# Performance work log

Hardware: AMD Instinct MI355X
Metric: run time of the kernel (lower is better)

## Reference

```python
import jax, jax.numpy as jnp
import numpy as np
import math

L, V, D, H, TBLK = 12, 50257, 768, 12, 1024
HD = D // H
EPS = 1e-5


def setup_inputs() -> dict:
    key = jax.random.key(0)
    ks = jax.random.split(key, 16)
    B, T = 2, 1024
    s = 0.02
    idx = jax.random.randint(ks[0], (B, T), 0, V, dtype=jnp.int32)
    inp = {
        "idx": idx,
        "wte": jax.random.normal(ks[1], (V, D), jnp.float32) * s,
        "wpe": jax.random.normal(ks[2], (TBLK, D), jnp.float32) * s,
        # per-layer params stacked along leading L axis
        "ln1_g": jnp.ones((L, D), jnp.float32),
        "ln1_b": jnp.zeros((L, D), jnp.float32),
        "attn_w": jax.random.normal(ks[3], (L, D, 3 * D), jnp.float32) * s,
        "attn_b": jnp.zeros((L, 3 * D), jnp.float32),
        "aproj_w": jax.random.normal(ks[4], (L, D, D), jnp.float32) * s,
        "aproj_b": jnp.zeros((L, D), jnp.float32),
        "ln2_g": jnp.ones((L, D), jnp.float32),
        "ln2_b": jnp.zeros((L, D), jnp.float32),
        "fc_w": jax.random.normal(ks[5], (L, D, 4 * D), jnp.float32) * s,
        "fc_b": jnp.zeros((L, 4 * D), jnp.float32),
        "mproj_w": jax.random.normal(ks[6], (L, 4 * D, D), jnp.float32) * s,
        "mproj_b": jnp.zeros((L, D), jnp.float32),
        "lnf_g": jnp.ones((D,), jnp.float32),
        "lnf_b": jnp.zeros((D,), jnp.float32),
        "lm_w": jax.random.normal(ks[7], (D, V), jnp.float32) * s,  # lm_head weight (stored transposed)
    }
    return inp


def _layer_norm(x, g, b):
    mu = jnp.mean(x, axis=-1, keepdims=True)
    var = jnp.mean(jnp.square(x - mu), axis=-1, keepdims=True)
    return (x - mu) * jax.lax.rsqrt(var + EPS) * g + b


def _block(x, p):
    (ln1g, ln1b, aw, ab, pw, pb, ln2g, ln2b, fw, fb, mw, mb) = p
    B, T, C = x.shape
    h = _layer_norm(x, ln1g, ln1b)
    qkv = h @ aw + ab  # [B,T,3D]
    q, k, v = jnp.split(qkv, 3, axis=-1)
    q = q.reshape(B, T, H, HD)
    k = k.reshape(B, T, H, HD)
    v = v.reshape(B, T, H, HD)
    scores = jnp.einsum('bihd,bjhd->bhij', q, k) * (1.0 / math.sqrt(HD))
    mask = jnp.tril(jnp.ones((T, T), bool))
    scores = jnp.where(mask, scores, jnp.float32(-jnp.inf))
    attn = jax.nn.softmax(scores, axis=-1)
    o = jnp.einsum('bhij,bjhd->bihd', attn, v).reshape(B, T, C)
    x = x + o @ pw + pb
    h = _layer_norm(x, ln2g, ln2b)
    h = jax.nn.gelu(h @ fw + fb, approximate=True)
    x = x + h @ mw + mb
    return x, None


def reference(idx, wte, wpe, ln1_g, ln1_b, attn_w, attn_b, aproj_w, aproj_b,
              ln2_g, ln2_b, fc_w, fc_b, mproj_w, mproj_b, lnf_g, lnf_b, lm_w):
    B, T = idx.shape
    x = wte[idx] + wpe[jnp.arange(T)]
    layers = (ln1_g, ln1_b, attn_w, attn_b, aproj_w, aproj_b,
              ln2_g, ln2_b, fc_w, fc_b, mproj_w, mproj_b)
    x, _ = jax.lax.scan(_block, x, layers)
    x = _layer_norm(x, lnf_g, lnf_b)
    logits = x @ lm_w  # [B,T,V]
    return logits
```

## Files before the change

### kernel.cpp

```cpp
#include <hip/hip_runtime.h>
#include <hip/hip_bf16.h>
#include <math.h>

#define BT_   2048
#define D_    768
#define T_    1024
#define H_    12
#define HD_   64
#define L_    12
#define V_    50257
#define VPAD_ 50304
#define NCHUNK_ 7168

typedef __hip_bfloat16 bf16;
typedef short bf16x8 __attribute__((ext_vector_type(8)));
typedef float f32x4 __attribute__((ext_vector_type(4)));

__global__ __launch_bounds__(256) void embed_kernel(const int* __restrict__ idx,
                                                    const float* __restrict__ wte,
                                                    const float* __restrict__ wpe,
                                                    float* __restrict__ x) {
    int bt = blockIdx.x;
    int t  = bt & (T_ - 1);
    int tok = idx[bt];
    const float* wrow = wte + (size_t)tok * D_;
    const float* prow = wpe + (size_t)t * D_;
    float* xrow = x + (size_t)bt * D_;
    for (int d = threadIdx.x; d < D_; d += 256)
        xrow[d] = wrow[d] + prow[d];
}

__global__ __launch_bounds__(256) void lnorm_kernel(const float* __restrict__ in,
                                                    const float* __restrict__ g,
                                                    const float* __restrict__ b,
                                                    bf16* __restrict__ out) {
    int row = blockIdx.x;
    const float* xr = in + (size_t)row * D_;
    float s = 0.f, s2 = 0.f;
    for (int d = threadIdx.x; d < D_; d += 256) {
        float v = xr[d];
        s += v; s2 += v * v;
    }
    #pragma unroll
    for (int o = 32; o >= 1; o >>= 1) {
        s  += __shfl_xor(s,  o);
        s2 += __shfl_xor(s2, o);
    }
    __shared__ float ss[4], ss2[4];
    int wid = threadIdx.x >> 6;
    if ((threadIdx.x & 63) == 0) { ss[wid] = s; ss2[wid] = s2; }
    __syncthreads();
    s  = ss[0] + ss[1] + ss[2] + ss[3];
    s2 = ss2[0] + ss2[1] + ss2[2] + ss2[3];
    float mu  = s / D_;
    float var = s2 / D_ - mu * mu;
    float rstd = rsqrtf(var + 1e-5f);
    bf16* orow = out + (size_t)row * D_;
    for (int d = threadIdx.x; d < D_; d += 256)
        orow[d] = __float2bfloat16((xr[d] - mu) * rstd * g[d] + b[d]);
}

__global__ __launch_bounds__(256) void convT_kernel(const float* __restrict__ W,
                                                    bf16* __restrict__ Wt,
                                                    int K, int ldW, int n_src0, int Nreal,
                                                    size_t sW, size_t sT) {
    W  += (size_t)blockIdx.z * sW;
    Wt += (size_t)blockIdx.z * sT;
    __shared__ float t[32][33];
    int tx = threadIdx.x & 31, ty = threadIdx.x >> 5;
    int k0 = blockIdx.y * 32, n0 = blockIdx.x * 32;
    #pragma unroll
    for (int i = 0; i < 4; i++) {
        int k = k0 + ty + i * 8;
        int n = n_src0 + n0 + tx;
        t[ty + i * 8][tx] = (n < Nreal) ? W[(size_t)k * ldW + n] : 0.f;
    }
    __syncthreads();
    #pragma unroll
    for (int i = 0; i < 4; i++)
        Wt[(size_t)(n0 + ty + i * 8) * K + k0 + tx] = __float2bfloat16(t[tx][ty + i * 8]);
}

__device__ inline float gelu_f(float v) {
    const float c = 0.7978845608028654f;
    float u = c * (v + 0.044715f * v * v * v);
    return 0.5f * v * (1.f + tanhf(u));
}

__device__ inline void gload16(const void* g, void* l) {
    __builtin_amdgcn_global_load_lds((const __attribute__((address_space(1))) void*)g,
                                     (__attribute__((address_space(3))) void*)l, 16, 0, 0);
}

template <int BM, int BN, int WM, int WN, int EPI, typename OT>
__device__ __attribute__((always_inline)) void gemm_body(
        const bf16* __restrict__ A, const bf16* __restrict__ Bt,
        const float* __restrict__ bias, const float* res, OT* C,
        int K, int ldC, int n_off, int Ncap, int nx) {
    constexpr int NW = WM * WN;
    constexpr int MI = BM / WM / 16;
    constexpr int NJ = BN / WN / 16;
    constexpr int GA = (BM / 16) / NW;
    constexpr int GB = (BN / 16) / NW;
    constexpr int G  = GA + GB;
    static_assert(GA >= 1 && GB >= 1, "stage mapping needs >=1 seg per wave");
    __shared__ __align__(16) short smem[3 * (BM + BN) * 32];
    short* Asm = smem;
    short* Bsm = smem + 3 * BM * 32;
    const int tid  = threadIdx.x;
    const int lane = tid & 63;
    const int wid  = tid >> 6;
    const int wm = wid / WN, wn = wid % WN;

    const int nwg = gridDim.x;
    const int bid = blockIdx.x;
    const int q8  = nwg >> 3, r8 = nwg & 7;
    const int xcd = bid & 7, off = bid >> 3;
    const int swz = (xcd < r8 ? xcd * (q8 + 1) : r8 * (q8 + 1) + (xcd - r8) * q8) + off;
    const int m0 = (swz % nx) * BM;
    const int n0 = (swz / nx) * BN;

    const int rS = lane >> 2;
    const int cS = ((lane & 3) ^ ((lane >> 3) & 3)) * 8;
    const int fr = lane & 15;
    const int fq = lane >> 4;
    const int rc = (fq ^ ((fr >> 1) & 3)) * 8;

    auto STAGE = [&](int buf, int k0) {
        #pragma unroll
        for (int s = 0; s < GA; s++) {
            const int seg = wid * GA + s;
            gload16(A + (size_t)(m0 + seg * 16 + rS) * K + k0 + cS, &Asm[buf * BM * 32 + seg * 512]);
        }
        #pragma unroll
        for (int s = 0; s < GB; s++) {
            const int seg = wid * GB + s;
            gload16(Bt + (size_t)(n0 + seg * 16 + rS) * K + k0 + cS, &Bsm[buf * BN * 32 + seg * 512]);
        }
    };

    f32x4 acc[MI][NJ] = {};

    auto COMPUTE = [&](int buf) {
        bf16x8 af[MI], bfr[NJ];
        #pragma unroll
        for (int i = 0; i < MI; i++)
            af[i] = *(const bf16x8*)&Asm[buf * BM * 32 + (wm * (BM / WM) + i * 16 + fr) * 32 + rc];
        #pragma unroll
        for (int j = 0; j < NJ; j++)
            bfr[j] = *(const bf16x8*)&Bsm[buf * BN * 32 + (wn * (BN / WN) + j * 16 + fr) * 32 + rc];
        #pragma unroll
        for (int i = 0; i < MI; i++)
            #pragma unroll
            for (int j = 0; j < NJ; j++)
                acc[i][j] = __builtin_amdgcn_mfma_f32_16x16x32_bf16(af[i], bfr[j], acc[i][j], 0, 0, 0);
    };

    const int nk = K / 32;
    STAGE(0, 0);
    STAGE(1, 32);
    int cur = 0;
    for (int ks = 0; ks < nk - 1; ks++) {
        asm volatile("s_waitcnt vmcnt(%0)" :: "n"(G) : "memory");
        __builtin_amdgcn_s_barrier();
        __builtin_amdgcn_sched_barrier(0);
        if (ks + 2 < nk) {
            int nxt = cur + 2; if (nxt >= 3) nxt -= 3;
            STAGE(nxt, (ks + 2) * 32);
        }
        COMPUTE(cur);
        cur = (cur + 1 == 3) ? 0 : cur + 1;
    }
    asm volatile("s_waitcnt vmcnt(0)" ::: "memory");
    __builtin_amdgcn_s_barrier();
    __builtin_amdgcn_sched_barrier(0);
    COMPUTE(cur);

    #pragma unroll
    for (int j = 0; j < NJ; j++) {
        const int col = n_off + n0 + wn * (BN / WN) + j * 16 + fr;
        if (col >= Ncap) continue;
        const float bb = (EPI == 3) ? 0.f : bias[col];
        #pragma unroll
        for (int i = 0; i < MI; i++) {
            #pragma unroll
            for (int r = 0; r < 4; r++) {
                const int row = m0 + wm * (BM / WM) + i * 16 + fq * 4 + r;
                float v = acc[i][j][r] + bb;
                if (EPI == 1) v += res[(size_t)row * ldC + col];
                if (EPI == 2) v = gelu_f(v);
                if constexpr (sizeof(OT) == 2)
                    C[(size_t)row * ldC + col] = __float2bfloat16(v);
                else
                    C[(size_t)row * ldC + col] = v;
            }
        }
    }
}

__global__ __launch_bounds__(256) void gemm_qkv(const bf16* A, const bf16* Bt, const float* bias,
                                                const float* res, bf16* C, int K, int ldC,
                                                int n_off, int Ncap, int nx) {
    gemm_body<128, 64, 2, 2, 0, bf16>(A, Bt, bias, res, C, K, ldC, n_off, Ncap, nx);
}
__global__ __launch_bounds__(256) void gemm_aproj(const bf16* A, const bf16* Bt, const float* bias,
                                                  const float* res, float* C, int K, int ldC,
                                                  int n_off, int Ncap, int nx) {
    gemm_body<64, 64, 2, 2, 1, float>(A, Bt, bias, res, C, K, ldC, n_off, Ncap, nx);
}
__global__ __launch_bounds__(256) void gemm_fc(const bf16* A, const bf16* Bt, const float* bias,
                                               const float* res, bf16* C, int K, int ldC,
                                               int n_off, int Ncap, int nx) {
    gemm_body<128, 64, 2, 2, 2, bf16>(A, Bt, bias, res, C, K, ldC, n_off, Ncap, nx);
}
__global__ __launch_bounds__(256) void gemm_mproj(const bf16* A, const bf16* Bt, const float* bias,
                                                  const float* res, float* C, int K, int ldC,
                                                  int n_off, int Ncap, int nx) {
    gemm_body<64, 64, 2, 2, 1, float>(A, Bt, bias, res, C, K, ldC, n_off, Ncap, nx);
}
__global__ __launch_bounds__(512) void gemm_lmhead(const bf16* A, const bf16* Bt, const float* bias,
                                                   const float* res, float* C, int K, int ldC,
                                                   int n_off, int Ncap, int nx) {
    gemm_body<128, 128, 4, 2, 3, float>(A, Bt, bias, res, C, K, ldC, n_off, Ncap, nx);
}

__device__ inline unsigned pk_bf16(float a, float b) {
    __hip_bfloat16 ha = __float2bfloat16(a), hb = __float2bfloat16(b);
    unsigned short ua = *(unsigned short*)&ha, ub = *(unsigned short*)&hb;
    return (unsigned)ua | ((unsigned)ub << 16);
}

__global__ __launch_bounds__(256) void fattn_kernel(const bf16* __restrict__ qkv,
                                                    bf16* __restrict__ att) {
    const int qi  = 15 - blockIdx.x;
    const int bh  = blockIdx.y;
    const int h   = bh % H_;
    const int b   = bh / H_;
    const int q0  = qi * 64;
    const int tid = threadIdx.x;
    const int lane = tid & 63;
    const int w   = tid >> 6;
    const int fr  = lane & 15;
    const int fq  = lane >> 4;

    __shared__ __align__(16) short K_lds[64 * 64];
    __shared__ __align__(16) short Vt_lds[64 * 64];
    __shared__ __align__(16) short P_lds[4][16 * 80];

    const size_t base = (size_t)b * T_ * 2304;
    const int qrow = q0 + w * 16 + fr;

    bf16x8 qf[2];
    qf[0] = *(const bf16x8*)(qkv + base + (size_t)qrow * 2304 + h * 64 + fq * 8);
    qf[1] = *(const bf16x8*)(qkv + base + (size_t)qrow * 2304 + h * 64 + 32 + fq * 8);

    const int vj  = tid >> 2;
    const int vd0 = (tid & 3) * 16;

    f32x4 acc[4] = {};
    float m = -1e30f, l = 0.f;

    const int nt = qi + 1;
    for (int kt = 0; kt < nt; kt++) {
        const int j0 = kt * 64;

        #pragma unroll
        for (int p = 0; p < 2; p++) {
            const int jl  = p * 32 + w * 8 + (lane >> 3);
            const int chg = (lane & 7) ^ (jl & 7);
            gload16(qkv + base + (size_t)(j0 + jl) * 2304 + D_ + h * 64 + chg * 8,
                    &K_lds[(p * 32 + w * 8) * 64]);
        }
        {
            const bf16* vsrc = qkv + base + (size_t)(j0 + vj) * 2304 + 2 * D_ + h * 64 + vd0;
            bf16x8 v0 = *(const bf16x8*)vsrc;
            bf16x8 v1 = *(const bf16x8*)(vsrc + 8);
            #pragma unroll
            for (int e = 0; e < 8; e++) {
                Vt_lds[((vd0 + e) * 64 + vj) ^ (e << 3)]     = v0[e];
                Vt_lds[((vd0 + 8 + e) * 64 + vj) ^ (e << 3)] = v1[e];
            }
        }
        __syncthreads();

        f32x4 s[4];
        #pragma unroll
        for (int jb = 0; jb < 4; jb++) {
            const int j = jb * 16 + fr;
            bf16x8 k0 = *(const bf16x8*)&K_lds[j * 64 + (((0 + fq) ^ (fr & 7)) << 3)];
            bf16x8 k1 = *(const bf16x8*)&K_lds[j * 64 + (((4 + fq) ^ (fr & 7)) << 3)];
            f32x4 z = {};
            z = __builtin_amdgcn_mfma_f32_16x16x32_bf16(k0, qf[0], z, 0, 0, 0);
            s[jb] = __builtin_amdgcn_mfma_f32_16x16x32_bf16(k1, qf[1], z, 0, 0, 0);
        }

        const bool need_mask = (j0 + 63 > q0 + w * 16);
        float mx = -1e30f;
        #pragma unroll
        for (int jb = 0; jb < 4; jb++) {
            #pragma unroll
            for (int r = 0; r < 4; r++) {
                float v = s[jb][r] * 0.125f;
                if (need_mask && (j0 + jb * 16 + fq * 4 + r > qrow)) v = -1e30f;
                s[jb][r] = v;
                mx = fmaxf(mx, v);
            }
        }
        mx = fmaxf(mx, __shfl_xor(mx, 16));
        mx = fmaxf(mx, __shfl_xor(mx, 32));

        const float mnew  = fmaxf(m, mx);
        const float alpha = __expf(m - mnew);

        float ts = 0.f;
        #pragma unroll
        for (int jb = 0; jb < 4; jb++) {
            #pragma unroll
            for (int r = 0; r < 4; r++) {
                s[jb][r] = __expf(s[jb][r] - mnew);
                ts += s[jb][r];
            }
            *(unsigned*)&P_lds[w][fr * 80 + jb * 16 + fq * 4]     = pk_bf16(s[jb][0], s[jb][1]);
            *(unsigned*)&P_lds[w][fr * 80 + jb * 16 + fq * 4 + 2] = pk_bf16(s[jb][2], s[jb][3]);
        }
        ts += __shfl_xor(ts, 16);
        ts += __shfl_xor(ts, 32);
        l = l * alpha + ts;
        #pragma unroll
        for (int db = 0; db < 4; db++)
            #pragma unroll
            for (int r = 0; r < 4; r++) acc[db][r] *= alpha;
        m = mnew;

        bf16x8 pa0 = *(const bf16x8*)&P_lds[w][fr * 80 + fq * 8];
        bf16x8 pa1 = *(const bf16x8*)&P_lds[w][fr * 80 + 32 + fq * 8];
        #pragma unroll
        for (int db = 0; db < 4; db++) {
            const int d = db * 16 + fr;
            bf16x8 vt0 = *(const bf16x8*)&Vt_lds[(d * 64 + fq * 8) ^ ((fr & 7) << 3)];
            bf16x8 vt1 = *(const bf16x8*)&Vt_lds[(d * 64 + 32 + fq * 8) ^ ((fr & 7) << 3)];
            acc[db] = __builtin_amdgcn_mfma_f32_16x16x32_bf16(vt0, pa0, acc[db], 0, 0, 0);
            acc[db] = __builtin_amdgcn_mfma_f32_16x16x32_bf16(vt1, pa1, acc[db], 0, 0, 0);
        }
        __syncthreads();
    }

    const float inv_l = 1.f / l;
    bf16* orow = att + (size_t)(b * T_ + qrow) * D_ + h * 64;
    #pragma unroll
    for (int db = 0; db < 4; db++) {
        #pragma unroll
        for (int rp = 0; rp < 2; rp++) {
            unsigned u = pk_bf16(acc[db][rp * 2] * inv_l, acc[db][rp * 2 + 1] * inv_l);
            *(unsigned*)(orow + db * 16 + fq * 4 + rp * 2) = u;
        }
    }
}

extern "C" void kernel_launch(void* const* d_in, const int* in_sizes, int n_in,
                              void* d_out, int out_size, void* d_ws, size_t ws_size,
                              hipStream_t stream) {
    const int* idx      = (const int*)  d_in[0];
    const float* wte    = (const float*)d_in[1];
    const float* wpe    = (const float*)d_in[2];
    const float* ln1_g  = (const float*)d_in[3];
    const float* ln1_b  = (const float*)d_in[4];
    const float* attn_w = (const float*)d_in[5];
    const float* attn_b = (const float*)d_in[6];
    const float* aproj_w= (const float*)d_in[7];
    const float* aproj_b= (const float*)d_in[8];
    const float* ln2_g  = (const float*)d_in[9];
    const float* ln2_b  = (const float*)d_in[10];
    const float* fc_w   = (const float*)d_in[11];
    const float* fc_b   = (const float*)d_in[12];
    const float* mproj_w= (const float*)d_in[13];
    const float* mproj_b= (const float*)d_in[14];
    const float* lnf_g  = (const float*)d_in[15];
    const float* lnf_b  = (const float*)d_in[16];
    const float* lm_w   = (const float*)d_in[17];
    float* out = (float*)d_out;

    char* wsB = (char*)d_ws;
    float* x   = (float*)(wsB);
    bf16*  big = (bf16*) (wsB + 6291456);
    bf16*  hbuf= (bf16*) (wsB + 18874368);
    bf16*  att = (bf16*) (wsB + 22020096);

    const size_t S_QKV = (size_t)2304 * 768, S_AP = (size_t)768 * 768;
    const size_t S_FC  = (size_t)3072 * 768, S_MP = (size_t)3072 * 768;
    const bool big_ws = ws_size >= 272302080ull;

    embed_kernel<<<BT_, 256, 0, stream>>>(idx, wte, wpe, x);

    if (big_ws) {
        bf16* w_qkv  = (bf16*)(wsB + 25165824);
        bf16* w_ap   = w_qkv + S_QKV * L_;
        bf16* w_fc   = w_ap  + S_AP  * L_;
        bf16* w_mp   = w_fc  + S_FC  * L_;
        bf16* lm_wt  = w_mp  + S_MP  * L_;

        convT_kernel<<<dim3(72, 24, L_), 256, 0, stream>>>(attn_w, w_qkv, 768, 2304, 0, 2304, S_QKV, S_QKV);
        convT_kernel<<<dim3(24, 24, L_), 256, 0, stream>>>(aproj_w, w_ap, 768, 768, 0, 768, S_AP, S_AP);
        convT_kernel<<<dim3(96, 24, L_), 256, 0, stream>>>(fc_w, w_fc, 768, 3072, 0, 3072, S_FC, S_FC);
        convT_kernel<<<dim3(24, 96, L_), 256, 0, stream>>>(mproj_w, w_mp, 3072, 768, 0, 768, S_MP, S_MP);
        convT_kernel<<<dim3(VPAD_ / 32, 24, 1), 256, 0, stream>>>(lm_w, lm_wt, 768, V_, 0, V_, 0, 0);

        for (int l = 0; l < L_; l++) {
            lnorm_kernel<<<BT_, 256, 0, stream>>>(x, ln1_g + (size_t)l * D_, ln1_b + (size_t)l * D_, hbuf);
            gemm_qkv<<<16 * 36, 256, 0, stream>>>(
                hbuf, w_qkv + l * S_QKV, attn_b + (size_t)l * 3 * D_, nullptr, big, 768, 2304, 0, 2304, 16);
            fattn_kernel<<<dim3(16, 2 * H_), 256, 0, stream>>>(big, att);
            gemm_aproj<<<32 * 12, 256, 0, stream>>>(
                att, w_ap + l * S_AP, aproj_b + (size_t)l * D_, x, x, 768, 768, 0, 768, 32);
            lnorm_kernel<<<BT_, 256, 0, stream>>>(x, ln2_g + (size_t)l * D_, ln2_b + (size_t)l * D_, hbuf);
            gemm_fc<<<16 * 48, 256, 0, stream>>>(
                hbuf, w_fc + l * S_FC, fc_b + (size_t)l * 4 * D_, nullptr, big, 768, 3072, 0, 3072, 16);
            gemm_mproj<<<32 * 12, 256, 0, stream>>>(
                big, w_mp + l * S_MP, mproj_b + (size_t)l * D_, x, x, 3072, 768, 0, 768, 32);
        }

        lnorm_kernel<<<BT_, 256, 0, stream>>>(x, lnf_g, lnf_b, hbuf);
        gemm_lmhead<<<16 * (VPAD_ / 128), 512, 0, stream>>>(
            hbuf, lm_wt, nullptr, nullptr, out, 768, V_, 0, V_, 16);
    } else {
        bf16* wbuf    = (bf16*)(wsB + 25165824);
        bf16* w_qkv   = wbuf;
        bf16* w_ap    = wbuf + S_QKV;
        bf16* w_fc    = w_ap + S_AP;
        bf16* w_mp    = w_fc + S_FC;

        for (int l = 0; l < L_; l++) {
            lnorm_kernel<<<BT_, 256, 0, stream>>>(x, ln1_g + (size_t)l * D_, ln1_b + (size_t)l * D_, hbuf);
            convT_kernel<<<dim3(72, 24, 1), 256, 0, stream>>>(
                attn_w + l * S_QKV, w_qkv, 768, 2304, 0, 2304, 0, 0);
            gemm_qkv<<<16 * 36, 256, 0, stream>>>(
                hbuf, w_qkv, attn_b + (size_t)l * 3 * D_, nullptr, big, 768, 2304, 0, 2304, 16);
            fattn_kernel<<<dim3(16, 2 * H_), 256, 0, stream>>>(big, att);
            convT_kernel<<<dim3(24, 24, 1), 256, 0, stream>>>(
                aproj_w + l * S_AP, w_ap, 768, 768, 0, 768, 0, 0);
            gemm_aproj<<<32 * 12, 256, 0, stream>>>(
                att, w_ap, aproj_b + (size_t)l * D_, x, x, 768, 768, 0, 768, 32);
            lnorm_kernel<<<BT_, 256, 0, stream>>>(x, ln2_g + (size_t)l * D_, ln2_b + (size_t)l * D_, hbuf);
            convT_kernel<<<dim3(96, 24, 1), 256, 0, stream>>>(
                fc_w + l * S_FC, w_fc, 768, 3072, 0, 3072, 0, 0);
            gemm_fc<<<16 * 48, 256, 0, stream>>>(
                hbuf, w_fc, fc_b + (size_t)l * 4 * D_, nullptr, big, 768, 3072, 0, 3072, 16);
            convT_kernel<<<dim3(24, 96, 1), 256, 0, stream>>>(
                mproj_w + l * S_MP, w_mp, 3072, 768, 0, 768, 0, 0);
            gemm_mproj<<<32 * 12, 256, 0, stream>>>(
                big, w_mp, mproj_b + (size_t)l * D_, x, x, 3072, 768, 0, 768, 32);
        }

        lnorm_kernel<<<BT_, 256, 0, stream>>>(x, lnf_g, lnf_b, hbuf);
        for (int c0 = 0; c0 < VPAD_; c0 += NCHUNK_) {
            int ncnt = (VPAD_ - c0 < NCHUNK_) ? (VPAD_ - c0) : NCHUNK_;
            convT_kernel<<<dim3(ncnt / 32, 24, 1), 256, 0, stream>>>(
                lm_w, wbuf, 768, V_, c0, V_, 0, 0);
            gemm_lmhead<<<16 * (ncnt / 128), 512, 0, stream>>>(
                hbuf, wbuf, nullptr, nullptr, out, 768, V_, c0, V_, 16);
        }
    }
}
```

Baseline: 2.178 ms.

## Replace LDS-staged layer GEMMs with register-direct MFMA GEMMs and smaller tiles

Adds a GEMM body that loads A and B fragments straight from global memory into registers, triple-buffered across K steps, with no LDS staging or barriers. The per-layer QKV, attention-projection, FC and MLP-projection GEMMs now use it with smaller tiles (64x64 and 32x64, the latter with 128-thread blocks), which doubles the grid size. The aim is to remove LDS traffic and synchronisation and to fill more CUs. In exchange each operand is reused less per workgroup, so more global and L2 traffic, and the fragment loads are only 16 bytes per lane. The LM head still uses the LDS-based kernel.

```diff
diff --git a/kernel.cpp b/kernel.cpp
--- a/kernel.cpp
+++ b/kernel.cpp
@@ -90,6 +90,102 @@
 __device__ inline void gload16(const void* g, void* l) {
     __builtin_amdgcn_global_load_lds((const __attribute__((address_space(1))) void*)g,
                                      (__attribute__((address_space(3))) void*)l, 16, 0, 0);
+}
+
+template <int BM, int BN, int WM, int WN, int EPI, typename OT>
+__device__ __attribute__((always_inline)) void reg_gemm_body(
+        const bf16* __restrict__ A, const bf16* __restrict__ Bt,
+        const float* __restrict__ bias, const float* res, OT* C,
+        int K, int ldC, int nx) {
+    constexpr int MI = BM / WM / 16;
+    constexpr int NJ = BN / WN / 16;
+    const int tid  = threadIdx.x;
+    const int lane = tid & 63;
+    const int wid  = tid >> 6;
+    const int wm = wid / WN, wn = wid % WN;
+    const int fr = lane & 15;
+    const int fq = lane >> 4;
+
+    const int nwg = gridDim.x;
+    const int bid = blockIdx.x;
+    const int q8  = nwg >> 3, r8 = nwg & 7;
+    const int xcd = bid & 7, off = bid >> 3;
+    const int swz = (xcd < r8 ? xcd * (q8 + 1) : r8 * (q8 + 1) + (xcd - r8) * q8) + off;
+    const int m0 = (swz % nx) * BM;
+    const int n0 = (swz / nx) * BN;
+
+    const bf16* Ap[MI];
+    const bf16* Bp[NJ];
+    #pragma unroll
+    for (int i = 0; i < MI; i++)
+        Ap[i] = A + (size_t)(m0 + wm * (BM / WM) + i * 16 + fr) * K + fq * 8;
+    #pragma unroll
+    for (int j = 0; j < NJ; j++)
+        Bp[j] = Bt + (size_t)(n0 + wn * (BN / WN) + j * 16 + fr) * K + fq * 8;
+
+    f32x4 acc[MI][NJ] = {};
+    bf16x8 a0[MI], b0[NJ], a1[MI], b1[NJ], a2[MI], b2[NJ];
+
+    auto LOADS = [&](bf16x8 (&aS)[MI], bf16x8 (&bS)[NJ], int off_e) {
+        #pragma unroll
+        for (int i = 0; i < MI; i++) aS[i] = *(const bf16x8*)(Ap[i] + off_e);
+        #pragma unroll
+        for (int j = 0; j < NJ; j++) bS[j] = *(const bf16x8*)(Bp[j] + off_e);
+    };
+    auto MM = [&](bf16x8 (&aS)[MI], bf16x8 (&bS)[NJ]) {
+        #pragma unroll
+        for (int i = 0; i < MI; i++)
+            #pragma unroll
+            for (int j = 0; j < NJ; j++)
+                acc[i][j] = __builtin_amdgcn_mfma_f32_16x16x32_bf16(aS[i], bS[j], acc[i][j], 0, 0, 0);
+    };
+
+    const int nk = K / 32;
+    LOADS(a0, b0, 0);
+    LOADS(a1, b1, 32);
+    LOADS(a2, b2, 64);
+    for (int ks = 0; ks < nk; ks += 3) {
+        MM(a0, b0); if (ks + 3 < nk) LOADS(a0, b0, (ks + 3) * 32);
+        MM(a1, b1); if (ks + 4 < nk) LOADS(a1, b1, (ks + 4) * 32);
+        MM(a2, b2); if (ks + 5 < nk) LOADS(a2, b2, (ks + 5) * 32);
+    }
+
+    #pragma unroll
+    for (int j = 0; j < NJ; j++) {
+        const int col = n0 + wn * (BN / WN) + j * 16 + fr;
+        const float bb = (EPI == 3) ? 0.f : bias[col];
+        #pragma unroll
+        for (int i = 0; i < MI; i++) {
+            #pragma unroll
+            for (int r = 0; r < 4; r++) {
+                const int row = m0 + wm * (BM / WM) + i * 16 + fq * 4 + r;
+                float v = acc[i][j][r] + bb;
+                if (EPI == 1) v += res[(size_t)row * ldC + col];
+                if (EPI == 2) v = gelu_f(v);
+                if constexpr (sizeof(OT) == 2)
+                    C[(size_t)row * ldC + col] = __float2bfloat16(v);
+                else
+                    C[(size_t)row * ldC + col] = v;
+            }
+        }
+    }
+}
+
+__global__ __launch_bounds__(256) void gemm_qkv(const bf16* A, const bf16* Bt, const float* bias,
+                                                const float* res, bf16* C, int K, int ldC, int nx) {
+    reg_gemm_body<64, 64, 2, 2, 0, bf16>(A, Bt, bias, res, C, K, ldC, nx);
+}
+__global__ __launch_bounds__(128) void gemm_aproj(const bf16* A, const bf16* Bt, const float* bias,
+                                                  const float* res, float* C, int K, int ldC, int nx) {
+    reg_gemm_body<32, 64, 1, 2, 1, float>(A, Bt, bias, res, C, K, ldC, nx);
+}
+__global__ __launch_bounds__(256) void gemm_fc(const bf16* A, const bf16* Bt, const float* bias,
+                                               const float* res, bf16* C, int K, int ldC, int nx) {
+    reg_gemm_body<64, 64, 2, 2, 2, bf16>(A, Bt, bias, res, C, K, ldC, nx);
+}
+__global__ __launch_bounds__(128) void gemm_mproj(const bf16* A, const bf16* Bt, const float* bias,
+                                                  const float* res, float* C, int K, int ldC, int nx) {
+    reg_gemm_body<32, 64, 1, 2, 1, float>(A, Bt, bias, res, C, K, ldC, nx);
 }
 
 template <int BM, int BN, int WM, int WN, int EPI, typename OT>
@@ -198,26 +294,6 @@
     }
 }
 
-__global__ __launch_bounds__(256) void gemm_qkv(const bf16* A, const bf16* Bt, const float* bias,
-                                                const float* res, bf16* C, int K, int ldC,
-                                                int n_off, int Ncap, int nx) {
-    gemm_body<128, 64, 2, 2, 0, bf16>(A, Bt, bias, res, C, K, ldC, n_off, Ncap, nx);
-}
-__global__ __launch_bounds__(256) void gemm_aproj(const bf16* A, const bf16* Bt, const float* bias,
-                                                  const float* res, float* C, int K, int ldC,
-                                                  int n_off, int Ncap, int nx) {
-    gemm_body<64, 64, 2, 2, 1, float>(A, Bt, bias, res, C, K, ldC, n_off, Ncap, nx);
-}
-__global__ __launch_bounds__(256) void gemm_fc(const bf16* A, const bf16* Bt, const float* bias,
-                                               const float* res, bf16* C, int K, int ldC,
-                                               int n_off, int Ncap, int nx) {
-    gemm_body<128, 64, 2, 2, 2, bf16>(A, Bt, bias, res, C, K, ldC, n_off, Ncap, nx);
-}
-__global__ __launch_bounds__(256) void gemm_mproj(const bf16* A, const bf16* Bt, const float* bias,
-                                                  const float* res, float* C, int K, int ldC,
-                                                  int n_off, int Ncap, int nx) {
-    gemm_body<64, 64, 2, 2, 1, float>(A, Bt, bias, res, C, K, ldC, n_off, Ncap, nx);
-}
 __global__ __launch_bounds__(512) void gemm_lmhead(const bf16* A, const bf16* Bt, const float* bias,
                                                    const float* res, float* C, int K, int ldC,
                                                    int n_off, int Ncap, int nx) {
@@ -407,16 +483,16 @@
 
         for (int l = 0; l < L_; l++) {
             lnorm_kernel<<<BT_, 256, 0, stream>>>(x, ln1_g + (size_t)l * D_, ln1_b + (size_t)l * D_, hbuf);
-            gemm_qkv<<<16 * 36, 256, 0, stream>>>(
-                hbuf, w_qkv + l * S_QKV, attn_b + (size_t)l * 3 * D_, nullptr, big, 768, 2304, 0, 2304, 16);
+            gemm_qkv<<<32 * 36, 256, 0, stream>>>(
+                hbuf, w_qkv + l * S_QKV, attn_b + (size_t)l * 3 * D_, nullptr, big, 768, 2304, 32);
             fattn_kernel<<<dim3(16, 2 * H_), 256, 0, stream>>>(big, att);
-            gemm_aproj<<<32 * 12, 256, 0, stream>>>(
-                att, w_ap + l * S_AP, aproj_b + (size_t)l * D_, x, x, 768, 768, 0, 768, 32);
+            gemm_aproj<<<64 * 12, 128, 0, stream>>>(
+                att, w_ap + l * S_AP, aproj_b + (size_t)l * D_, x, x, 768, 768, 64);
             lnorm_kernel<<<BT_, 256, 0, stream>>>(x, ln2_g + (size_t)l * D_, ln2_b + (size_t)l * D_, hbuf);
-            gemm_fc<<<16 * 48, 256, 0, stream>>>(
-                hbuf, w_fc + l * S_FC, fc_b + (size_t)l * 4 * D_, nullptr, big, 768, 3072, 0, 3072, 16);
-            gemm_mproj<<<32 * 12, 256, 0, stream>>>(
-                big, w_mp + l * S_MP, mproj_b + (size_t)l * D_, x, x, 3072, 768, 0, 768, 32);
+            gemm_fc<<<32 * 48, 256, 0, stream>>>(
+                hbuf, w_fc + l * S_FC, fc_b + (size_t)l * 4 * D_, nullptr, big, 768, 3072, 32);
+            gemm_mproj<<<64 * 12, 128, 0, stream>>>(
+                big, w_mp + l * S_MP, mproj_b + (size_t)l * D_, x, x, 3072, 768, 64);
         }
 
         lnorm_kernel<<<BT_, 256, 0, stream>>>(x, lnf_g, lnf_b, hbuf);
@@ -433,22 +509,22 @@
             lnorm_kernel<<<BT_, 256, 0, stream>>>(x, ln1_g + (size_t)l * D_, ln1_b + (size_t)l * D_, hbuf);
             convT_kernel<<<dim3(72, 24, 1), 256, 0, stream>>>(
                 attn_w + l * S_QKV, w_qkv, 768, 2304, 0, 2304, 0, 0);
-            gemm_qkv<<<16 * 36, 256, 0, stream>>>(
-                hbuf, w_qkv, attn_b + (size_t)l * 3 * D_, nullptr, big, 768, 2304, 0, 2304, 16);
+            gemm_qkv<<<32 * 36, 256, 0, stream>>>(
+                hbuf, w_qkv, attn_b + (size_t)l * 3 * D_, nullptr, big, 768, 2304, 32);
             fattn_kernel<<<dim3(16, 2 * H_), 256, 0, stream>>>(big, att);
             convT_kernel<<<dim3(24, 24, 1), 256, 0, stream>>>(
                 aproj_w + l * S_AP, w_ap, 768, 768, 0, 768, 0, 0);
-            gemm_aproj<<<32 * 12, 256, 0, stream>>>(
-                att, w_ap, aproj_b + (size_t)l * D_, x, x, 768, 768, 0, 768, 32);
+            gemm_aproj<<<64 * 12, 128, 0, stream>>>(
+                att, w_ap, aproj_b + (size_t)l * D_, x, x, 768, 768, 64);
             lnorm_kernel<<<BT_, 256, 0, stream>>>(x, ln2_g + (size_t)l * D_, ln2_b + (size_t)l * D_, hbuf);
             convT_kernel<<<dim3(96, 24, 1), 256, 0, stream>>>(
                 fc_w + l * S_FC, w_fc, 768, 3072, 0, 3072, 0, 0);
-            gemm_fc<<<16 * 48, 256, 0, stream>>>(
-                hbuf, w_fc, fc_b + (size_t)l * 4 * D_, nullptr, big, 768, 3072, 0, 3072, 16);
+            gemm_fc<<<32 * 48, 256, 0, stream>>>(
+                hbuf, w_fc, fc_b + (size_t)l * 4 * D_, nullptr, big, 768, 3072, 32);
             convT_kernel<<<dim3(24, 96, 1), 256, 0, stream>>>(
                 mproj_w + l * S_MP, w_mp, 3072, 768, 0, 768, 0, 0);
-            gemm_mproj<<<32 * 12, 256, 0, stream>>>(
-                big, w_mp, mproj_b + (size_t)l * D_, x, x, 3072, 768, 0, 768, 32);
+            gemm_mproj<<<64 * 12, 128, 0, stream>>>(
+                big, w_mp, mproj_b + (size_t)l * D_, x, x, 3072, 768, 64);
         }
 
         lnorm_kernel<<<BT_, 256, 0, stream>>>(x, lnf_g, lnf_b, hbuf);
```

Result: slower. 3.699 ms (+69.8%).
